# Performance work log

Hardware: AMD Instinct MI355X
Metric: run time of the kernel (lower is better)

The kernel has to match this reference:

```python
import jax, jax.numpy as jnp
import numpy as np

N = 200000          # real (non-pad) faces
P = 8192            # pad entries
PAD = N + P         # padded table size
C_IN = 128
C_OUT = 128


def setup_inputs() -> dict:
    key = jax.random.key(0)
    ks = jax.random.split(key, 6)
    x = jax.random.normal(ks[0], (N, C_IN), jnp.float32)
    # column 0 = the face itself (a real, non-pad index); columns 1..8 = neighbors
    col0 = jnp.arange(N, dtype=jnp.int64)[:, None]
    nbrs = jax.random.randint(ks[1], (N, 8), 0, PAD, dtype=jnp.int64)
    face_neighborhood = jnp.concatenate([col0, nbrs], axis=1)
    face_is_pad = jnp.arange(PAD) >= N  # last P rows are padding
    s = 1.0 / np.sqrt(C_IN).astype(np.float32)
    in_proj_w = jax.random.normal(ks[2], (3 * C_IN, C_IN), jnp.float32) * s
    in_proj_b = jnp.zeros((3 * C_IN,), jnp.float32)
    out_proj_w = jax.random.normal(ks[3], (C_IN, C_IN), jnp.float32) * s
    out_proj_b = jnp.zeros((C_IN,), jnp.float32)
    conv_w = jax.random.normal(ks[4], (C_OUT, C_IN, 1, 2), jnp.float32) * (1.0 / np.sqrt(2.0 * C_IN).astype(np.float32))
    conv_b = jnp.zeros((C_OUT,), jnp.float32)
    return {
        "x": x,
        "face_neighborhood": face_neighborhood,
        "face_is_pad": face_is_pad,
        "pad_size": PAD,
        "in_proj_w": in_proj_w,
        "in_proj_b": in_proj_b,
        "out_proj_w": out_proj_w,
        "out_proj_b": out_proj_b,
        "conv_w": conv_w,
        "conv_b": conv_b,
    }


def reference(x, face_neighborhood, face_is_pad, pad_size,
              in_proj_w, in_proj_b, out_proj_w, out_proj_b, conv_w, conv_b):
    C = x.shape[1]
    H = max(1, C // 32)
    Dh = C // H
    # scatter real features into the padded table (padded_x[~face_is_pad] = x)
    nonpad_idx = jnp.nonzero(~face_is_pad, size=x.shape[0])[0]
    padded_x = jnp.zeros((pad_size, C), x.dtype).at[nonpad_idx].set(x)
    f = padded_x[face_neighborhood]              # [N, 9, C] 9-way gather
    center = f[:, 0]                             # [N, C] query feature
    kv = f[:, 1:]                                # [N, 8, C]
    # torch MultiheadAttention: packed in_proj then per-head scaled dot-product
    q = (center @ in_proj_w[:C].T + in_proj_b[:C]).reshape(-1, 1, H, Dh).transpose(0, 2, 1, 3)       # [N,H,1,Dh]
    k = (kv @ in_proj_w[C:2 * C].T + in_proj_b[C:2 * C]).reshape(-1, 8, H, Dh).transpose(0, 2, 1, 3)  # [N,H,8,Dh]
    v = (kv @ in_proj_w[2 * C:].T + in_proj_b[2 * C:]).reshape(-1, 8, H, Dh).transpose(0, 2, 1, 3)    # [N,H,8,Dh]
    scale = 1.0 / jnp.sqrt(jnp.asarray(Dh, q.dtype))
    scores = jnp.einsum('nhqd,nhkd->nhqk', q, k) * scale  # [N,H,1,8]
    pad_mask = face_is_pad[face_neighborhood[:, 1:]][:, None, None, :]  # [N,1,1,8]
    scores = jnp.where(pad_mask, -jnp.inf, scores)
    attn = jax.nn.softmax(scores, axis=-1)
    o = jnp.einsum('nhqk,nhkd->nhqd', attn, v)            # [N,H,1,Dh]
    o = o.transpose(0, 2, 1, 3).reshape(-1, C)            # [N,C] (q_len==1)
    h = o @ out_proj_w.T + out_proj_b                     # [N,C]
    # Conv2d(C_in, C_out, (1,2)) over [N, C, 1, 2] == linear fuse of center & h
    out = center @ conv_w[:, :, 0, 0].T + h @ conv_w[:, :, 0, 1].T + conv_b  # [N, C_out]
    return out
```

## Files before the change

kernel.cpp:

```cpp
#include <hip/hip_runtime.h>

typedef __bf16 bfrag __attribute__((ext_vector_type(8)));
typedef float f32x4 __attribute__((ext_vector_type(4)));

__device__ __forceinline__ unsigned short f2bf(float f) {
  unsigned u = __float_as_uint(f);
  u = (u + 0x7fffu + ((u >> 16) & 1u)) >> 16;
  return (unsigned short)u;
}
__device__ __forceinline__ float bflo(unsigned u) { return __uint_as_float(u << 16); }
__device__ __forceinline__ float bfhi(unsigned u) { return __uint_as_float(u & 0xffff0000u); }

__global__ void k_prep(const float* __restrict__ in_proj_w,
                       const float* __restrict__ conv_w,
                       const float* __restrict__ out_proj_w,
                       const float* __restrict__ out_proj_b,
                       const float* __restrict__ conv_b,
                       unsigned short* __restrict__ WcatF,
                       unsigned short* __restrict__ W2F,
                       float* __restrict__ cvec) {
  int b = blockIdx.x, t = threadIdx.x;
  if (b < 384) {
    unsigned short v = f2bf(in_proj_w[b * 128 + t]);
    int cb = b >> 7, r7 = b & 127;
    int cB = r7 >> 4, mr = r7 & 15;
    int ks = t >> 5, quad = (t >> 3) & 3, j = t & 7;
    WcatF[(((cb * 8 + cB) * 4 + ks) << 9) + (quad * 16 + mr) * 8 + j] = v;
    return;
  }
  const int c = b - 384;
  const int cB = c >> 4, mr = c & 15;
  __shared__ float cw[128];
  __shared__ float red[2];
  cw[t] = conv_w[(c * 128 + t) * 2 + 1];
  __syncthreads();

  float a[8] = {0.f, 0.f, 0.f, 0.f, 0.f, 0.f, 0.f, 0.f};
#pragma unroll
  for (int kk = 0; kk < 16; ++kk)
#pragma unroll
    for (int u = 0; u < 8; ++u)
      a[u] += cw[kk * 8 + u] * out_proj_w[(kk * 8 + u) * 128 + t];
  float s = ((a[0] + a[1]) + (a[2] + a[3])) + ((a[4] + a[5]) + (a[6] + a[7]));

  {
    int kc = t >> 6, ks2 = (t >> 5) & 1, quad = (t >> 3) & 3, j = t & 7;
    W2F[(((cB * 4 + kc) * 2 + ks2) << 9) + (quad * 16 + mr) * 8 + j] = f2bf(s);
  }
  {
    int K = 128 + t;
    int kc = K >> 6, ks2 = (K >> 5) & 1, quad = (K >> 3) & 3, j = K & 7;
    W2F[(((cB * 4 + kc) * 2 + ks2) << 9) + (quad * 16 + mr) * 8 + j] =
        f2bf(conv_w[(c * 128 + t) * 2]);
  }

  float p = cw[t] * out_proj_b[t];
#pragma unroll
  for (int d = 1; d < 64; d <<= 1) p += __shfl_xor(p, d);
  if ((t & 63) == 0) red[t >> 6] = p;
  __syncthreads();
  if (t == 0) cvec[c] = conv_b[c] + red[0] + red[1];
}

__global__ __launch_bounds__(256, 4) void k_gemm_qkv(
    const float* __restrict__ x, const unsigned short* __restrict__ WcatF,
    const float* __restrict__ in_proj_b, unsigned short* __restrict__ Qb,
    unsigned short* __restrict__ KVb, int M) {
  __shared__ unsigned short se[4][32 * 72];
  const int m0 = blockIdx.x * 128;
  const int t = threadIdx.x;
  const int w = t >> 6, lane = t & 63, quad = lane >> 4, mr = lane & 15;
  unsigned short* sew = se[w];

  bfrag af[4][2];
#pragma unroll
  for (int ks = 0; ks < 4; ++ks)
#pragma unroll
    for (int r = 0; r < 2; ++r) {
      int row = m0 + w * 32 + r * 16 + mr;
      union { unsigned short s[8]; bfrag f; } u;
      if (row < M) {
        const float4* p =
            reinterpret_cast<const float4*>(&x[(size_t)row * 128 + ks * 32 + quad * 8]);
        float4 v0 = p[0], v1 = p[1];
        u.s[0] = f2bf(v0.x); u.s[1] = f2bf(v0.y); u.s[2] = f2bf(v0.z); u.s[3] = f2bf(v0.w);
        u.s[4] = f2bf(v1.x); u.s[5] = f2bf(v1.y); u.s[6] = f2bf(v1.z); u.s[7] = f2bf(v1.w);
      } else {
#pragma unroll
        for (int i = 0; i < 8; ++i) u.s[i] = 0;
      }
      af[ks][r] = u.f;
    }

#pragma unroll
  for (int cb = 0; cb < 3; ++cb) {
    unsigned short* dst = (cb == 0) ? Qb : KVb;
    const int ldst = (cb == 0) ? 128 : 256;
    const int cb_off = (cb == 2) ? 128 : 0;
#pragma unroll
    for (int half = 0; half < 2; ++half) {
      f32x4 acc[2][4];
#pragma unroll
      for (int r = 0; r < 2; ++r)
#pragma unroll
        for (int c = 0; c < 4; ++c) acc[r][c] = (f32x4){0.f, 0.f, 0.f, 0.f};
#pragma unroll
      for (int ks = 0; ks < 4; ++ks)
#pragma unroll
        for (int c = 0; c < 4; ++c) {
          union { uint4 v; bfrag f; } u;
          u.v = *reinterpret_cast<const uint4*>(
              &WcatF[(((cb * 8 + half * 4 + c) * 4 + ks) << 9) + lane * 8]);
          acc[0][c] = __builtin_amdgcn_mfma_f32_16x16x32_bf16(af[ks][0], u.f, acc[0][c], 0, 0, 0);
          acc[1][c] = __builtin_amdgcn_mfma_f32_16x16x32_bf16(af[ks][1], u.f, acc[1][c], 0, 0, 0);
        }
      const float* bias = in_proj_b + cb * 128 + half * 64;
#pragma unroll
      for (int r = 0; r < 2; ++r)
#pragma unroll
        for (int c = 0; c < 4; ++c) {
          float bv = bias[c * 16 + mr];
#pragma unroll
          for (int g = 0; g < 4; ++g)
            sew[(r * 16 + quad * 4 + g) * 72 + c * 16 + mr] = f2bf(acc[r][c][g] + bv);
        }
#pragma unroll
      for (int i = 0; i < 4; ++i) {
        int ch = i * 64 + lane;
        int row = ch >> 3, cp = ch & 7;
        int grow = m0 + w * 32 + row;
        if (grow < M) {
          uint4 v = *reinterpret_cast<const uint4*>(&sew[row * 72 + cp * 8]);
          *reinterpret_cast<uint4*>(
              &dst[(size_t)grow * ldst + cb_off + half * 64 + cp * 8]) = v;
        }
      }
    }
  }
}

__global__ __launch_bounds__(256) void k_attn_out(
    const unsigned short* __restrict__ Qb, const unsigned short* __restrict__ KVb,
    const int* __restrict__ fn, const float* __restrict__ x,
    const unsigned short* __restrict__ W2F, const float* __restrict__ cvec,
    float* __restrict__ out, int M) {
  __shared__ char smem[18432];
  unsigned short* Ow = reinterpret_cast<unsigned short*>(smem);
  const int base = blockIdx.x * 32;
  const int t = threadIdx.x;
  const int w = t >> 6, lane = t & 63, quad = lane >> 4, mr = lane & 15;
  const int hf = lane >> 5, l5 = lane & 31;
  const float scale = 0.17677669529663687f;

  for (int it = 0; it < 4; ++it) {
    const int ri = it * 8 + w * 2 + hf;
    const int n = base + ri;
    union { unsigned short s[4]; uint2 u; } pk;
    pk.u = make_uint2(0u, 0u);
    if (n < M) {
      unsigned long long q8 = __builtin_nontemporal_load(
          reinterpret_cast<const unsigned long long*>(&Qb[(size_t)n * 128 + 4 * l5]));
      float q0 = bflo((unsigned)q8), q1 = bfhi((unsigned)q8);
      float q2 = bflo((unsigned)(q8 >> 32)), q3 = bfhi((unsigned)(q8 >> 32));
      int idx[8];
#pragma unroll
      for (int j = 0; j < 8; ++j)
        idx[j] = __builtin_nontemporal_load(&fn[n * 9 + 1 + j]);
      float o0 = 0.f, o1 = 0.f, o2 = 0.f, o3 = 0.f, sum = 0.f;
#pragma unroll
      for (int j = 0; j < 8; ++j) {
        bool valid = idx[j] < M;
        int id = valid ? idx[j] : 0;
        const unsigned short* rowp = &KVb[(size_t)id * 256 + 4 * l5];
        uint2 kk = *reinterpret_cast<const uint2*>(rowp);
        uint2 vv = *reinterpret_cast<const uint2*>(rowp + 128);
        float k0 = bflo(kk.x), k1 = bfhi(kk.x), k2 = bflo(kk.y), k3 = bfhi(kk.y);
        float p = q0 * k0 + q1 * k1 + q2 * k2 + q3 * k3;
        p += __shfl_xor(p, 1);
        p += __shfl_xor(p, 2);
        p += __shfl_xor(p, 4);
        float s = valid ? p * scale : -1e30f;
        float e = __expf(s);
        sum += e;
        float v0 = bflo(vv.x), v1 = bfhi(vv.x), v2 = bflo(vv.y), v3 = bfhi(vv.y);
        o0 += e * v0; o1 += e * v1; o2 += e * v2; o3 += e * v3;
      }
      float inv = 1.f / sum;
      pk.s[0] = f2bf(o0 * inv); pk.s[1] = f2bf(o1 * inv);
      pk.s[2] = f2bf(o2 * inv); pk.s[3] = f2bf(o3 * inv);
    }
    *reinterpret_cast<uint2*>(&Ow[ri * 136 + 4 * l5]) = pk.u;
  }
  __syncthreads();

  f32x4 acc[2][2];
#pragma unroll
  for (int r = 0; r < 2; ++r)
#pragma unroll
    for (int c = 0; c < 2; ++c) acc[r][c] = (f32x4){0.f, 0.f, 0.f, 0.f};

#pragma unroll
  for (int kc = 0; kc < 4; ++kc) {
    bfrag af[2][2];
#pragma unroll
    for (int ks2 = 0; ks2 < 2; ++ks2)
#pragma unroll
      for (int r = 0; r < 2; ++r) {
        if (kc < 2) {
          union { uint4 v; bfrag f; } u;
          u.v = *reinterpret_cast<const uint4*>(
              &Ow[(r * 16 + mr) * 136 + kc * 64 + ks2 * 32 + quad * 8]);
          af[ks2][r] = u.f;
        } else {
          int row = base + r * 16 + mr;
          union { unsigned short s[8]; bfrag f; } u;
          if (row < M) {
            const float4* p = reinterpret_cast<const float4*>(
                &x[(size_t)row * 128 + (kc - 2) * 64 + ks2 * 32 + quad * 8]);
            float4 v0 = p[0], v1 = p[1];
            u.s[0] = f2bf(v0.x); u.s[1] = f2bf(v0.y); u.s[2] = f2bf(v0.z); u.s[3] = f2bf(v0.w);
            u.s[4] = f2bf(v1.x); u.s[5] = f2bf(v1.y); u.s[6] = f2bf(v1.z); u.s[7] = f2bf(v1.w);
          } else {
#pragma unroll
            for (int i = 0; i < 8; ++i) u.s[i] = 0;
          }
          af[ks2][r] = u.f;
        }
      }
#pragma unroll
    for (int ks2 = 0; ks2 < 2; ++ks2)
#pragma unroll
      for (int c2 = 0; c2 < 2; ++c2) {
        union { uint4 v; bfrag f; } u;
        u.v = *reinterpret_cast<const uint4*>(
            &W2F[((((w * 2 + c2) * 4 + kc) * 2 + ks2) << 9) + lane * 8]);
        acc[0][c2] = __builtin_amdgcn_mfma_f32_16x16x32_bf16(af[ks2][0], u.f, acc[0][c2], 0, 0, 0);
        acc[1][c2] = __builtin_amdgcn_mfma_f32_16x16x32_bf16(af[ks2][1], u.f, acc[1][c2], 0, 0, 0);
      }
  }

  __syncthreads();
  float* sfw = reinterpret_cast<float*>(smem) + w * (32 * 36);
#pragma unroll
  for (int c2 = 0; c2 < 2; ++c2) {
    float cv = cvec[(w * 2 + c2) * 16 + mr];
#pragma unroll
    for (int r = 0; r < 2; ++r)
#pragma unroll
      for (int g = 0; g < 4; ++g)
        sfw[(r * 16 + quad * 4 + g) * 36 + c2 * 16 + mr] = acc[r][c2][g] + cv;
  }
#pragma unroll
  for (int i = 0; i < 4; ++i) {
    int ch = i * 64 + lane;
    int row = ch >> 3, c4 = ch & 7;
    int grow = base + row;
    if (grow < M) {
      float4 v = *reinterpret_cast<const float4*>(&sfw[row * 36 + c4 * 4]);
      *reinterpret_cast<float4*>(&out[(size_t)grow * 128 + w * 32 + c4 * 4]) = v;
    }
  }
}

__global__ __launch_bounds__(256) void k_attn(
    const unsigned short* __restrict__ Qb, const unsigned short* __restrict__ KVb,
    const int* __restrict__ fn, unsigned short* __restrict__ Ob, int M) {
  const int w = threadIdx.x >> 6, lane = threadIdx.x & 63;
  const int hf = lane >> 5, l5 = lane & 31;
  const int n = blockIdx.x * 8 + w * 2 + hf;
  if (n >= M) return;
  const float scale = 0.17677669529663687f;
  uint2 qp = *reinterpret_cast<const uint2*>(&Qb[(size_t)n * 128 + 4 * l5]);
  float q0 = bflo(qp.x), q1 = bfhi(qp.x), q2 = bflo(qp.y), q3 = bfhi(qp.y);
  int idx[8];
#pragma unroll
  for (int j = 0; j < 8; ++j) idx[j] = fn[n * 9 + 1 + j];
  float o0 = 0.f, o1 = 0.f, o2 = 0.f, o3 = 0.f, sum = 0.f;
#pragma unroll
  for (int j = 0; j < 8; ++j) {
    bool valid = idx[j] < M;
    int id = valid ? idx[j] : 0;
    const unsigned short* rowp = &KVb[(size_t)id * 256 + 4 * l5];
    uint2 kk = *reinterpret_cast<const uint2*>(rowp);
    uint2 vv = *reinterpret_cast<const uint2*>(rowp + 128);
    float k0 = bflo(kk.x), k1 = bfhi(kk.x), k2 = bflo(kk.y), k3 = bfhi(kk.y);
    float p = q0 * k0 + q1 * k1 + q2 * k2 + q3 * k3;
    p += __shfl_xor(p, 1);
    p += __shfl_xor(p, 2);
    p += __shfl_xor(p, 4);
    float s = valid ? p * scale : -1e30f;
    float e = __expf(s);
    sum += e;
    float v0 = bflo(vv.x), v1 = bfhi(vv.x), v2 = bflo(vv.y), v3 = bfhi(vv.y);
    o0 += e * v0; o1 += e * v1; o2 += e * v2; o3 += e * v3;
  }
  float inv = 1.f / sum;
  union { unsigned short s[4]; uint2 u; } pk;
  pk.s[0] = f2bf(o0 * inv); pk.s[1] = f2bf(o1 * inv);
  pk.s[2] = f2bf(o2 * inv); pk.s[3] = f2bf(o3 * inv);
  *reinterpret_cast<uint2*>(&Ob[(size_t)n * 128 + 4 * l5]) = pk.u;
}

__global__ __launch_bounds__(256, 4) void k_gemm_out(
    const unsigned short* __restrict__ Ob, const float* __restrict__ x,
    const unsigned short* __restrict__ W2F, const float* __restrict__ cvec,
    float* __restrict__ out, int M) {
  __shared__ float sf[4][32 * 36];
  const int m0 = blockIdx.x * 128;
  const int t = threadIdx.x;
  const int w = t >> 6, lane = t & 63, quad = lane >> 4, mr = lane & 15;
  float* sfw = sf[w];

  f32x4 acc[2][8];
#pragma unroll
  for (int r = 0; r < 2; ++r)
#pragma unroll
    for (int c = 0; c < 8; ++c) acc[r][c] = (f32x4){0.f, 0.f, 0.f, 0.f};

#pragma unroll
  for (int kc = 0; kc < 4; ++kc) {
    bfrag af[2][2];
#pragma unroll
    for (int ks2 = 0; ks2 < 2; ++ks2)
#pragma unroll
      for (int r = 0; r < 2; ++r) {
        int row = m0 + w * 32 + r * 16 + mr;
        if (kc < 2) {
          union { uint4 v; bfrag f; } u;
          u.v = make_uint4(0u, 0u, 0u, 0u);
          if (row < M)
            u.v = *reinterpret_cast<const uint4*>(
                &Ob[(size_t)row * 128 + kc * 64 + ks2 * 32 + quad * 8]);
          af[ks2][r] = u.f;
        } else {
          union { unsigned short s[8]; bfrag f; } u;
          if (row < M) {
            const float4* p = reinterpret_cast<const float4*>(
                &x[(size_t)row * 128 + (kc - 2) * 64 + ks2 * 32 + quad * 8]);
            float4 v0 = p[0], v1 = p[1];
            u.s[0] = f2bf(v0.x); u.s[1] = f2bf(v0.y); u.s[2] = f2bf(v0.z); u.s[3] = f2bf(v0.w);
            u.s[4] = f2bf(v1.x); u.s[5] = f2bf(v1.y); u.s[6] = f2bf(v1.z); u.s[7] = f2bf(v1.w);
          } else {
#pragma unroll
            for (int i = 0; i < 8; ++i) u.s[i] = 0;
          }
          af[ks2][r] = u.f;
        }
      }
#pragma unroll
    for (int ks2 = 0; ks2 < 2; ++ks2)
#pragma unroll
      for (int c = 0; c < 8; ++c) {
        union { uint4 v; bfrag f; } u;
        u.v = *reinterpret_cast<const uint4*>(
            &W2F[(((c * 4 + kc) * 2 + ks2) << 9) + lane * 8]);
        acc[0][c] = __builtin_amdgcn_mfma_f32_16x16x32_bf16(af[ks2][0], u.f, acc[0][c], 0, 0, 0);
        acc[1][c] = __builtin_amdgcn_mfma_f32_16x16x32_bf16(af[ks2][1], u.f, acc[1][c], 0, 0, 0);
      }
  }
#pragma unroll
  for (int p = 0; p < 4; ++p) {
#pragma unroll
    for (int cc = 0; cc < 2; ++cc) {
      int c = p * 2 + cc;
      float cv = cvec[c * 16 + mr];
#pragma unroll
      for (int r = 0; r < 2; ++r)
#pragma unroll
        for (int g = 0; g < 4; ++g)
          sfw[(r * 16 + quad * 4 + g) * 36 + cc * 16 + mr] = acc[r][c][g] + cv;
    }
#pragma unroll
    for (int i = 0; i < 4; ++i) {
      int ch = i * 64 + lane;
      int row = ch >> 3, c4 = ch & 7;
      int grow = m0 + w * 32 + row;
      if (grow < M) {
        float4 v = *reinterpret_cast<const float4*>(&sfw[row * 36 + c4 * 4]);
        *reinterpret_cast<float4*>(&out[(size_t)grow * 128 + p * 32 + c4 * 4]) = v;
      }
    }
  }
}

extern "C" void kernel_launch(void* const* d_in, const int* in_sizes, int n_in,
                              void* d_out, int out_size, void* d_ws, size_t ws_size,
                              hipStream_t stream) {
  const float* x          = (const float*)d_in[0];
  const int*   fn         = (const int*)d_in[1];
  const float* in_proj_w  = (const float*)d_in[4];
  const float* in_proj_b  = (const float*)d_in[5];
  const float* out_proj_w = (const float*)d_in[6];
  const float* out_proj_b = (const float*)d_in[7];
  const float* conv_w     = (const float*)d_in[8];
  const float* conv_b     = (const float*)d_in[9];
  const int M = in_sizes[0] / 128;
  const int mt = (M + 127) / 128;
  char* ws = (char*)d_ws;

  const size_t qbytes  = (size_t)M * 128 * 2;
  const size_t kvbytes = (size_t)M * 256 * 2;
  const size_t wbytes  = (size_t)(384 * 128 + 128 * 256) * 2 + 512;

  if (ws_size >= qbytes + kvbytes + wbytes) {
    unsigned short* Qb    = (unsigned short*)ws;
    unsigned short* KVb   = (unsigned short*)(ws + qbytes);
    unsigned short* WcatF = (unsigned short*)(ws + qbytes + kvbytes);
    unsigned short* W2F   = WcatF + 384 * 128;
    float*          cvec  = (float*)(W2F + 128 * 256);

    k_prep<<<dim3(512), dim3(128), 0, stream>>>(in_proj_w, conv_w, out_proj_w,
                                                out_proj_b, conv_b, WcatF, W2F, cvec);
    k_gemm_qkv<<<dim3(mt), dim3(256), 0, stream>>>(x, WcatF, in_proj_b, Qb, KVb, M);
    k_attn_out<<<dim3((M + 31) / 32), dim3(256), 0, stream>>>(
        Qb, KVb, fn, x, W2F, cvec, (float*)d_out, M);
  } else {
    unsigned short* KVb   = (unsigned short*)d_out;
    unsigned short* Qb    = (unsigned short*)ws;
    unsigned short* Ob    = (unsigned short*)(ws + (size_t)M * 128 * 2);
    unsigned short* WcatF = (unsigned short*)(ws + (size_t)M * 128 * 4);
    unsigned short* W2F   = WcatF + 384 * 128;
    float*          cvec  = (float*)(W2F + 128 * 256);

    k_prep<<<dim3(512), dim3(128), 0, stream>>>(in_proj_w, conv_w, out_proj_w,
                                                out_proj_b, conv_b, WcatF, W2F, cvec);
    k_gemm_qkv<<<dim3(mt), dim3(256), 0, stream>>>(x, WcatF, in_proj_b, Qb, KVb, M);
    k_attn<<<dim3((M + 7) / 8), dim3(256), 0, stream>>>(Qb, KVb, fn, Ob, M);
    k_gemm_out<<<dim3(mt), dim3(256), 0, stream>>>(Ob, x, W2F, cvec, (float*)d_out, M);
  }
}
```

Measured before the change: 402.1 us.

## Fuse Q projection into attention kernel, drop Q buffer round trip

The Q projection moves out of the QKV GEMM and into the attention/output kernel. Each block now converts its 32 rows of x to bf16 once, computes Q with MFMA into LDS, and reuses the same x fragments later for the conv center term. This removes the global write and read of the Q buffer and the second load of x. In exchange the attention kernel does more work and holds more registers before its gather phase, which may lower occupancy.

```diff
diff --git a/kernel.cpp b/kernel.cpp
--- a/kernel.cpp
+++ b/kernel.cpp
@@ -62,10 +62,9 @@
   if (t == 0) cvec[c] = conv_b[c] + red[0] + red[1];
 }
 
-__global__ __launch_bounds__(256, 4) void k_gemm_qkv(
+__global__ __launch_bounds__(256, 4) void k_gemm_kv(
     const float* __restrict__ x, const unsigned short* __restrict__ WcatF,
-    const float* __restrict__ in_proj_b, unsigned short* __restrict__ Qb,
-    unsigned short* __restrict__ KVb, int M) {
+    const float* __restrict__ in_proj_b, unsigned short* __restrict__ KVb, int M) {
   __shared__ unsigned short se[4][32 * 72];
   const int m0 = blockIdx.x * 128;
   const int t = threadIdx.x;
@@ -93,9 +92,7 @@
     }
 
 #pragma unroll
-  for (int cb = 0; cb < 3; ++cb) {
-    unsigned short* dst = (cb == 0) ? Qb : KVb;
-    const int ldst = (cb == 0) ? 128 : 256;
+  for (int cb = 1; cb < 3; ++cb) {
     const int cb_off = (cb == 2) ? 128 : 0;
 #pragma unroll
     for (int half = 0; half < 2; ++half) {
@@ -132,7 +129,7 @@
         if (grow < M) {
           uint4 v = *reinterpret_cast<const uint4*>(&sew[row * 72 + cp * 8]);
           *reinterpret_cast<uint4*>(
-              &dst[(size_t)grow * ldst + cb_off + half * 64 + cp * 8]) = v;
+              &KVb[(size_t)grow * 256 + cb_off + half * 64 + cp * 8]) = v;
         }
       }
     }
@@ -140,17 +137,67 @@
 }
 
 __global__ __launch_bounds__(256) void k_attn_out(
-    const unsigned short* __restrict__ Qb, const unsigned short* __restrict__ KVb,
-    const int* __restrict__ fn, const float* __restrict__ x,
-    const unsigned short* __restrict__ W2F, const float* __restrict__ cvec,
-    float* __restrict__ out, int M) {
+    const unsigned short* __restrict__ KVb, const int* __restrict__ fn,
+    const float* __restrict__ x, const unsigned short* __restrict__ WcatF,
+    const float* __restrict__ in_proj_b, const unsigned short* __restrict__ W2F,
+    const float* __restrict__ cvec, float* __restrict__ out, int M) {
   __shared__ char smem[18432];
-  unsigned short* Ow = reinterpret_cast<unsigned short*>(smem);
+  unsigned short* Qw = reinterpret_cast<unsigned short*>(smem);
+  unsigned short* Ow = reinterpret_cast<unsigned short*>(smem) + 32 * 136;
   const int base = blockIdx.x * 32;
   const int t = threadIdx.x;
   const int w = t >> 6, lane = t & 63, quad = lane >> 4, mr = lane & 15;
   const int hf = lane >> 5, l5 = lane & 31;
   const float scale = 0.17677669529663687f;
+
+  bfrag af[4][2];
+#pragma unroll
+  for (int ks = 0; ks < 4; ++ks)
+#pragma unroll
+    for (int r = 0; r < 2; ++r) {
+      int row = base + r * 16 + mr;
+      union { unsigned short s[8]; bfrag f; } u;
+      if (row < M) {
+        const float4* p =
+            reinterpret_cast<const float4*>(&x[(size_t)row * 128 + ks * 32 + quad * 8]);
+        float4 v0 = p[0], v1 = p[1];
+        u.s[0] = f2bf(v0.x); u.s[1] = f2bf(v0.y); u.s[2] = f2bf(v0.z); u.s[3] = f2bf(v0.w);
+        u.s[4] = f2bf(v1.x); u.s[5] = f2bf(v1.y); u.s[6] = f2bf(v1.z); u.s[7] = f2bf(v1.w);
+      } else {
+#pragma unroll
+        for (int i = 0; i < 8; ++i) u.s[i] = 0;
+      }
+      af[ks][r] = u.f;
+    }
+
+  {
+    f32x4 qacc[2][2];
+#pragma unroll
+    for (int r = 0; r < 2; ++r)
+#pragma unroll
+      for (int c2 = 0; c2 < 2; ++c2) qacc[r][c2] = (f32x4){0.f, 0.f, 0.f, 0.f};
+#pragma unroll
+    for (int ks = 0; ks < 4; ++ks)
+#pragma unroll
+      for (int c2 = 0; c2 < 2; ++c2) {
+        union { uint4 v; bfrag f; } u;
+        u.v = *reinterpret_cast<const uint4*>(
+            &WcatF[((((w * 2 + c2) * 4) + ks) << 9) + lane * 8]);
+        qacc[0][c2] = __builtin_amdgcn_mfma_f32_16x16x32_bf16(af[ks][0], u.f, qacc[0][c2], 0, 0, 0);
+        qacc[1][c2] = __builtin_amdgcn_mfma_f32_16x16x32_bf16(af[ks][1], u.f, qacc[1][c2], 0, 0, 0);
+      }
+#pragma unroll
+    for (int c2 = 0; c2 < 2; ++c2) {
+      float bv = in_proj_b[(w * 2 + c2) * 16 + mr];
+#pragma unroll
+      for (int r = 0; r < 2; ++r)
+#pragma unroll
+        for (int g = 0; g < 4; ++g)
+          Qw[(r * 16 + quad * 4 + g) * 136 + (w * 2 + c2) * 16 + mr] =
+              f2bf(qacc[r][c2][g] + bv);
+    }
+  }
+  __syncthreads();
 
   for (int it = 0; it < 4; ++it) {
     const int ri = it * 8 + w * 2 + hf;
@@ -158,10 +205,8 @@
     union { unsigned short s[4]; uint2 u; } pk;
     pk.u = make_uint2(0u, 0u);
     if (n < M) {
-      unsigned long long q8 = __builtin_nontemporal_load(
-          reinterpret_cast<const unsigned long long*>(&Qb[(size_t)n * 128 + 4 * l5]));
-      float q0 = bflo((unsigned)q8), q1 = bfhi((unsigned)q8);
-      float q2 = bflo((unsigned)(q8 >> 32)), q3 = bfhi((unsigned)(q8 >> 32));
+      uint2 qp = *reinterpret_cast<const uint2*>(&Qw[ri * 136 + 4 * l5]);
+      float q0 = bflo(qp.x), q1 = bfhi(qp.x), q2 = bflo(qp.y), q3 = bfhi(qp.y);
       int idx[8];
 #pragma unroll
       for (int j = 0; j < 8; ++j)
@@ -201,7 +246,7 @@
 
 #pragma unroll
   for (int kc = 0; kc < 4; ++kc) {
-    bfrag af[2][2];
+    bfrag a2[2][2];
 #pragma unroll
     for (int ks2 = 0; ks2 < 2; ++ks2)
 #pragma unroll
@@ -210,21 +255,9 @@
           union { uint4 v; bfrag f; } u;
           u.v = *reinterpret_cast<const uint4*>(
               &Ow[(r * 16 + mr) * 136 + kc * 64 + ks2 * 32 + quad * 8]);
-          af[ks2][r] = u.f;
+          a2[ks2][r] = u.f;
         } else {
-          int row = base + r * 16 + mr;
-          union { unsigned short s[8]; bfrag f; } u;
-          if (row < M) {
-            const float4* p = reinterpret_cast<const float4*>(
-                &x[(size_t)row * 128 + (kc - 2) * 64 + ks2 * 32 + quad * 8]);
-            float4 v0 = p[0], v1 = p[1];
-            u.s[0] = f2bf(v0.x); u.s[1] = f2bf(v0.y); u.s[2] = f2bf(v0.z); u.s[3] = f2bf(v0.w);
-            u.s[4] = f2bf(v1.x); u.s[5] = f2bf(v1.y); u.s[6] = f2bf(v1.z); u.s[7] = f2bf(v1.w);
-          } else {
-#pragma unroll
-            for (int i = 0; i < 8; ++i) u.s[i] = 0;
-          }
-          af[ks2][r] = u.f;
+          a2[ks2][r] = af[(kc - 2) * 2 + ks2][r];
         }
       }
 #pragma unroll
@@ -234,8 +267,8 @@
         union { uint4 v; bfrag f; } u;
         u.v = *reinterpret_cast<const uint4*>(
             &W2F[((((w * 2 + c2) * 4 + kc) * 2 + ks2) << 9) + lane * 8]);
-        acc[0][c2] = __builtin_amdgcn_mfma_f32_16x16x32_bf16(af[ks2][0], u.f, acc[0][c2], 0, 0, 0);
-        acc[1][c2] = __builtin_amdgcn_mfma_f32_16x16x32_bf16(af[ks2][1], u.f, acc[1][c2], 0, 0, 0);
+        acc[0][c2] = __builtin_amdgcn_mfma_f32_16x16x32_bf16(a2[ks2][0], u.f, acc[0][c2], 0, 0, 0);
+        acc[1][c2] = __builtin_amdgcn_mfma_f32_16x16x32_bf16(a2[ks2][1], u.f, acc[1][c2], 0, 0, 0);
       }
   }
 
@@ -258,6 +291,83 @@
     if (grow < M) {
       float4 v = *reinterpret_cast<const float4*>(&sfw[row * 36 + c4 * 4]);
       *reinterpret_cast<float4*>(&out[(size_t)grow * 128 + w * 32 + c4 * 4]) = v;
+    }
+  }
+}
+
+__global__ __launch_bounds__(256, 4) void k_gemm_qkv(
+    const float* __restrict__ x, const unsigned short* __restrict__ WcatF,
+    const float* __restrict__ in_proj_b, unsigned short* __restrict__ Qb,
+    unsigned short* __restrict__ KVb, int M) {
+  __shared__ unsigned short se[4][32 * 72];
+  const int m0 = blockIdx.x * 128;
+  const int t = threadIdx.x;
+  const int w = t >> 6, lane = t & 63, quad = lane >> 4, mr = lane & 15;
+  unsigned short* sew = se[w];
+
+  bfrag af[4][2];
+#pragma unroll
+  for (int ks = 0; ks < 4; ++ks)
+#pragma unroll
+    for (int r = 0; r < 2; ++r) {
+      int row = m0 + w * 32 + r * 16 + mr;
+      union { unsigned short s[8]; bfrag f; } u;
+      if (row < M) {
+        const float4* p =
+            reinterpret_cast<const float4*>(&x[(size_t)row * 128 + ks * 32 + quad * 8]);
+        float4 v0 = p[0], v1 = p[1];
+        u.s[0] = f2bf(v0.x); u.s[1] = f2bf(v0.y); u.s[2] = f2bf(v0.z); u.s[3] = f2bf(v0.w);
+        u.s[4] = f2bf(v1.x); u.s[5] = f2bf(v1.y); u.s[6] = f2bf(v1.z); u.s[7] = f2bf(v1.w);
+      } else {
+#pragma unroll
+        for (int i = 0; i < 8; ++i) u.s[i] = 0;
+      }
+      af[ks][r] = u.f;
+    }
+
+#pragma unroll
+  for (int cb = 0; cb < 3; ++cb) {
+    unsigned short* dst = (cb == 0) ? Qb : KVb;
+    const int ldst = (cb == 0) ? 128 : 256;
+    const int cb_off = (cb == 2) ? 128 : 0;
+#pragma unroll
+    for (int half = 0; half < 2; ++half) {
+      f32x4 acc[2][4];
+#pragma unroll
+      for (int r = 0; r < 2; ++r)
+#pragma unroll
+        for (int c = 0; c < 4; ++c) acc[r][c] = (f32x4){0.f, 0.f, 0.f, 0.f};
+#pragma unroll
+      for (int ks = 0; ks < 4; ++ks)
+#pragma unroll
+        for (int c = 0; c < 4; ++c) {
+          union { uint4 v; bfrag f; } u;
+          u.v = *reinterpret_cast<const uint4*>(
+              &WcatF[(((cb * 8 + half * 4 + c) * 4 + ks) << 9) + lane * 8]);
+          acc[0][c] = __builtin_amdgcn_mfma_f32_16x16x32_bf16(af[ks][0], u.f, acc[0][c], 0, 0, 0);
+          acc[1][c] = __builtin_amdgcn_mfma_f32_16x16x32_bf16(af[ks][1], u.f, acc[1][c], 0, 0, 0);
+        }
+      const float* bias = in_proj_b + cb * 128 + half * 64;
+#pragma unroll
+      for (int r = 0; r < 2; ++r)
+#pragma unroll
+        for (int c = 0; c < 4; ++c) {
+          float bv = bias[c * 16 + mr];
+#pragma unroll
+          for (int g = 0; g < 4; ++g)
+            sew[(r * 16 + quad * 4 + g) * 72 + c * 16 + mr] = f2bf(acc[r][c][g] + bv);
+        }
+#pragma unroll
+      for (int i = 0; i < 4; ++i) {
+        int ch = i * 64 + lane;
+        int row = ch >> 3, cp = ch & 7;
+        int grow = m0 + w * 32 + row;
+        if (grow < M) {
+          uint4 v = *reinterpret_cast<const uint4*>(&sew[row * 72 + cp * 8]);
+          *reinterpret_cast<uint4*>(
+              &dst[(size_t)grow * ldst + cb_off + half * 64 + cp * 8]) = v;
+        }
+      }
     }
   }
 }
@@ -398,22 +508,20 @@
   const int mt = (M + 127) / 128;
   char* ws = (char*)d_ws;
 
-  const size_t qbytes  = (size_t)M * 128 * 2;
   const size_t kvbytes = (size_t)M * 256 * 2;
   const size_t wbytes  = (size_t)(384 * 128 + 128 * 256) * 2 + 512;
 
-  if (ws_size >= qbytes + kvbytes + wbytes) {
-    unsigned short* Qb    = (unsigned short*)ws;
-    unsigned short* KVb   = (unsigned short*)(ws + qbytes);
-    unsigned short* WcatF = (unsigned short*)(ws + qbytes + kvbytes);
+  if (ws_size >= kvbytes + wbytes) {
+    unsigned short* KVb   = (unsigned short*)ws;
+    unsigned short* WcatF = (unsigned short*)(ws + kvbytes);
     unsigned short* W2F   = WcatF + 384 * 128;
     float*          cvec  = (float*)(W2F + 128 * 256);
 
     k_prep<<<dim3(512), dim3(128), 0, stream>>>(in_proj_w, conv_w, out_proj_w,
                                                 out_proj_b, conv_b, WcatF, W2F, cvec);
-    k_gemm_qkv<<<dim3(mt), dim3(256), 0, stream>>>(x, WcatF, in_proj_b, Qb, KVb, M);
+    k_gemm_kv<<<dim3(mt), dim3(256), 0, stream>>>(x, WcatF, in_proj_b, KVb, M);
     k_attn_out<<<dim3((M + 31) / 32), dim3(256), 0, stream>>>(
-        Qb, KVb, fn, x, W2F, cvec, (float*)d_out, M);
+        KVb, fn, x, WcatF, in_proj_b, W2F, cvec, (float*)d_out, M);
   } else {
     unsigned short* KVb   = (unsigned short*)d_out;
     unsigned short* Qb    = (unsigned short*)ws;
```

After: 398.8 us. Within noise of the previous version (-0.8%).
